# Performance work log

Hardware: AMD Instinct MI355X
Metric: run time of the kernel (lower is better)

## Reference

```python
import jax, jax.numpy as jnp
import numpy as np

N_NODES = 50000
N_EDGES = 600000
D = 128
EDGE_D = 32
N_LAYERS = 3
BN_EPS = 1e-5


def setup_inputs() -> dict:
    key = jax.random.key(0)
    ks = jax.random.split(key, 8)
    x = jax.random.normal(ks[0], (N_NODES, D), dtype=jnp.float32)
    edge_index = jax.random.randint(ks[1], (2, N_EDGES), 0, N_NODES, dtype=jnp.int64)
    edge_attr = jax.random.normal(ks[2], (N_EDGES, EDGE_D), dtype=jnp.float32)
    W_lin = jax.random.normal(ks[3], (N_LAYERS, EDGE_D, D), dtype=jnp.float32) * 0.05
    b_lin = jnp.zeros((N_LAYERS, D), dtype=jnp.float32)
    W1 = jax.random.normal(ks[4], (N_LAYERS, D, D), dtype=jnp.float32) * 0.05
    b1 = jnp.zeros((N_LAYERS, D), dtype=jnp.float32)
    W2 = jax.random.normal(ks[5], (N_LAYERS, D, D), dtype=jnp.float32) * 0.05
    b2 = jnp.zeros((N_LAYERS, D), dtype=jnp.float32)
    gamma = jnp.ones((N_LAYERS, D), dtype=jnp.float32)
    beta = jnp.zeros((N_LAYERS, D), dtype=jnp.float32)
    return {"x": x, "edge_index": edge_index, "edge_attr": edge_attr,
            "W_lin": W_lin, "b_lin": b_lin, "W1": W1, "b1": b1,
            "W2": W2, "b2": b2, "gamma": gamma, "beta": beta}


def reference(x, edge_index, edge_attr, W_lin, b_lin, W1, b1, W2, b2, gamma, beta):
    # MPNN with GINEConv layers: for each layer,
    #   msg_e = ReLU(x[src_e] + Linear(edge_attr_e))      (PyG GINEConv edge lift)
    #   agg_i = sum over edges with dst==i of msg_e        (scatter-sum)
    #   h     = MLP((1+eps)*x + agg), eps=0
    #   x     = ReLU(BatchNorm1d(h))                       (training-mode batch stats)
    src, dst = edge_index[0], edge_index[1]
    n = x.shape[0]
    for l in range(W1.shape[0]):
        e = edge_attr @ W_lin[l] + b_lin[l]                 # [E, D]
        msg = jax.nn.relu(x[src] + e)                       # gather + fuse
        agg = jax.ops.segment_sum(msg, dst, num_segments=n)  # [N, D]
        h = x + agg                                         # eps = 0
        h = jax.nn.relu(h @ W1[l] + b1[l]) @ W2[l] + b2[l]   # GIN MLP
        mu = jnp.mean(h, axis=0)
        var = jnp.var(h, axis=0)
        h = (h - mu) * jax.lax.rsqrt(var + BN_EPS) * gamma[l] + beta[l]
        x = jax.nn.relu(h)
    return x
```

## Files before the change

kernel.cpp:

```cpp
#include <hip/hip_runtime.h>

#define D_DIM 128
#define EDGE_DIM 32
#define BN_EPS 1e-5f

typedef __attribute__((ext_vector_type(8))) _Float16 f16x8;
typedef __attribute__((ext_vector_type(2))) _Float16 half2v;
typedef __attribute__((ext_vector_type(4))) float f32x4;
typedef unsigned short ushort_t;

__device__ __forceinline__ unsigned short f2h(float f) {
    union { _Float16 h; unsigned short u; } c;
    c.h = (_Float16)f;
    return c.u;
}
__device__ __forceinline__ unsigned pk2h(float lo, float hi) {
    return (unsigned)f2h(lo) | ((unsigned)f2h(hi) << 16);
}
__device__ __forceinline__ half2v asH2(unsigned u) {
    union { unsigned u; half2v h; } c;
    c.u = u;
    return c.h;
}
__device__ __forceinline__ float fdot2f(half2v a, half2v b, float c) {
#if __has_builtin(__builtin_amdgcn_fdot2)
    return __builtin_amdgcn_fdot2(a, b, c, false);
#else
    return c + (float)a.x * (float)b.x + (float)a.y * (float)b.y;
#endif
}

__global__ __launch_bounds__(256) void hist_kernel(
    const int* __restrict__ dst, int* __restrict__ cnt, int E)
{
    for (int e = blockIdx.x * 256 + threadIdx.x; e < E; e += gridDim.x * 256)
        atomicAdd(&cnt[dst[e]], 1);
}

__global__ __launch_bounds__(256) void scan_local_kernel(
    const int* __restrict__ cnt, int* __restrict__ off,
    int* __restrict__ blksum, int n)
{
    __shared__ int part[256];
    const int t = threadIdx.x;
    const int base = blockIdx.x * 2048 + t * 8;
    int v[8];
    int s = 0;
#pragma unroll
    for (int j = 0; j < 8; ++j) {
        const int idx = base + j;
        const int c = (idx < n) ? cnt[idx] : 0;
        v[j] = s;
        s += c;
    }
    part[t] = s;
    __syncthreads();
    for (int d = 1; d < 256; d <<= 1) {
        const int val = (t >= d) ? part[t - d] : 0;
        __syncthreads();
        part[t] += val;
        __syncthreads();
    }
    const int texcl = (t > 0) ? part[t - 1] : 0;
#pragma unroll
    for (int j = 0; j < 8; ++j) {
        const int idx = base + j;
        if (idx < n) off[idx] = texcl + v[j];
    }
    if (t == 255) blksum[blockIdx.x] = part[255];
}

__global__ __launch_bounds__(64) void scan_tops_kernel(
    int* __restrict__ blksum, int* __restrict__ off, int n, int B)
{
    if (threadIdx.x == 0) {
        int run = 0;
        for (int b = 0; b < B; ++b) {
            const int v = blksum[b];
            blksum[b] = run;
            run += v;
        }
        off[n] = run;
    }
}

__global__ __launch_bounds__(256) void scan_add_kernel(
    int* __restrict__ off, int* __restrict__ cur,
    const int* __restrict__ blksum, int n)
{
    const int base = blockIdx.x * 2048;
    const int add = blksum[blockIdx.x];
    for (int j = threadIdx.x; j < 2048; j += 256) {
        const int i = base + j;
        if (i < n) {
            const int v = off[i] + add;
            off[i] = v;
            cur[i] = v;
        }
    }
}

__global__ __launch_bounds__(256) void scatter_kernel(
    const int* __restrict__ src, const int* __restrict__ dst,
    int* __restrict__ cur, int* __restrict__ srcs,
    int* __restrict__ csr_eid, int E)
{
    for (int e = blockIdx.x * 256 + threadIdx.x; e < E; e += gridDim.x * 256) {
        const int p = atomicAdd(&cur[dst[e]], 1);
        srcs[p]    = src[e];
        csr_eid[p] = e;
    }
}

__global__ __launch_bounds__(256) void ea_permute_kernel(
    const float* __restrict__ ea, const int* __restrict__ csr_eid,
    uint4* __restrict__ ea16q, int E)
{
    const int idx = blockIdx.x * 256 + threadIdx.x;
    const int p = idx >> 2;
    if (p >= E) return;
    const int q = idx & 3;
    const int eid = csr_eid[p];
    const float4 a = *(const float4*)(ea + (size_t)eid * EDGE_DIM + q * 8);
    const float4 b = *(const float4*)(ea + (size_t)eid * EDGE_DIM + q * 8 + 4);
    uint4 o;
    o.x = pk2h(a.x, a.y); o.y = pk2h(a.z, a.w);
    o.z = pk2h(b.x, b.y); o.w = pk2h(b.z, b.w);
    ea16q[(size_t)p * 4 + q] = o;
}

__global__ __launch_bounds__(256) void wl_build_kernel(
    const float* __restrict__ Wl, unsigned* __restrict__ wl16d)
{
#pragma unroll
    for (int r = 0; r < 8; ++r) {
        const int idx = r * 256 + threadIdx.x;
        const int kp = idx >> 7, c = idx & 127;
        wl16d[idx] = pk2h(Wl[(2 * kp) * D_DIM + c], Wl[(2 * kp + 1) * D_DIM + c]);
    }
}

template<int XFORM>
__global__ __launch_bounds__(256) void xprep_kernel(
    const float* __restrict__ h, const float* __restrict__ scsh,
    uint2* __restrict__ x16q, int M)
{
    __shared__ float sc[128], sh[128];
    if (XFORM) {
        if (threadIdx.x < 128) {
            sc[threadIdx.x] = scsh[threadIdx.x];
            sh[threadIdx.x] = scsh[128 + threadIdx.x];
        }
        __syncthreads();
    }
    const int total = M * 32;
    for (int i = blockIdx.x * 256 + threadIdx.x; i < total; i += gridDim.x * 256) {
        float4 v = ((const float4*)h)[i];
        if (XFORM) {
            const int c = (i & 31) * 4;
            v.x = fmaxf(fmaf(v.x, sc[c + 0], sh[c + 0]), 0.f);
            v.y = fmaxf(fmaf(v.y, sc[c + 1], sh[c + 1]), 0.f);
            v.z = fmaxf(fmaf(v.z, sc[c + 2], sh[c + 2]), 0.f);
            v.w = fmaxf(fmaf(v.w, sc[c + 3], sh[c + 3]), 0.f);
        }
        uint2 o; o.x = pk2h(v.x, v.y); o.y = pk2h(v.z, v.w);
        x16q[i] = o;
    }
}

__global__ __launch_bounds__(256) void edge_agg_kernel(
    const unsigned* __restrict__ x16d,
    const int*      __restrict__ srcs,
    const uint4*    __restrict__ ea16q,
    const int*      __restrict__ row_off,
    const unsigned* __restrict__ wl16d,
    const float*    __restrict__ bl,
    float*          __restrict__ agg,
    int nNodes)
{
    const int lane = threadIdx.x & 63;
    const int wid  = threadIdx.x >> 6;

    unsigned wA[16], wB[16];
#pragma unroll
    for (int kp = 0; kp < 16; ++kp) {
        const uint2 w2 = *(const uint2*)(wl16d + kp * 128 + 2 * lane);
        wA[kp] = w2.x; wB[kp] = w2.y;
    }
    const float b0 = bl[2 * lane];
    const float b1 = bl[2 * lane + 1];

    const int stride = gridDim.x * 4;
    for (int node = blockIdx.x * 4 + wid; node < nNodes; node += stride) {
        const int beg = __builtin_amdgcn_readfirstlane(row_off[node]);
        const int end = __builtin_amdgcn_readfirstlane(row_off[node + 1]);
        float acc0 = 0.f, acc1 = 0.f;

        auto edge_body = [&](int p) {
            const int s = srcs[p];
            const uint4 q0 = ea16q[(size_t)p * 4 + 0];
            const uint4 q1 = ea16q[(size_t)p * 4 + 1];
            const uint4 q2 = ea16q[(size_t)p * 4 + 2];
            const uint4 q3 = ea16q[(size_t)p * 4 + 3];
            const unsigned xd = x16d[(size_t)s * 64 + lane];
            const unsigned aw[16] = {q0.x, q0.y, q0.z, q0.w,
                                     q1.x, q1.y, q1.z, q1.w,
                                     q2.x, q2.y, q2.z, q2.w,
                                     q3.x, q3.y, q3.z, q3.w};
            float e0 = b0, e1 = b1;
#pragma unroll
            for (int kp = 0; kp < 16; ++kp) {
                e0 = fdot2f(asH2(aw[kp]), asH2(wA[kp]), e0);
                e1 = fdot2f(asH2(aw[kp]), asH2(wB[kp]), e1);
            }
            const half2v xh = asH2(xd);
            acc0 += fmaxf((float)xh.x + e0, 0.f);
            acc1 += fmaxf((float)xh.y + e1, 0.f);
        };

        int j = beg;
        if ((end - beg) & 1) { edge_body(j); ++j; }
#pragma unroll 1
        for (; j < end; j += 2) {
            edge_body(j);
            edge_body(j + 1);
        }
        *(float2*)(agg + (size_t)node * D_DIM + 2 * lane) = make_float2(acc0, acc1);
    }
}

__global__ __launch_bounds__(256) void gemm1_kernel(
    const unsigned* __restrict__ x16d,
    const float* __restrict__ agg,
    const float* __restrict__ W,
    const float* __restrict__ bias,
    ushort_t* __restrict__ h1,
    int M)
{
    __shared__ char ATb[128 * 256];
    __shared__ char WTb[128 * 256];
    const int tid = threadIdx.x;
    const int m0  = blockIdx.x * 128;

#pragma unroll
    for (int i = 0; i < 16; ++i) {
        const int idx = i * 256 + tid;
        const int r = idx >> 5, c4 = idx & 31;
        const int row = m0 + r;
        f32x4 v = {0.f, 0.f, 0.f, 0.f};
        if (row < M) {
            const uint2 xv = *(const uint2*)(x16d + (size_t)row * 64 + c4 * 2);
            const f32x4 g  = *(const f32x4*)(agg + (size_t)row * 128 + c4 * 4);
            const half2v xa = asH2(xv.x), xb = asH2(xv.y);
            v[0] = (float)xa.x + g[0];
            v[1] = (float)xa.y + g[1];
            v[2] = (float)xb.x + g[2];
            v[3] = (float)xb.y + g[3];
        }
        uint2 p; p.x = pk2h(v[0], v[1]); p.y = pk2h(v[2], v[3]);
        *(uint2*)(ATb + r * 256 + ((c4 * 8) ^ ((r & 7) << 4))) = p;
    }
#pragma unroll
    for (int i = 0; i < 8; ++i) {
        const int c4 = (tid >> 6) + 4 * i;
        const int kp = tid & 63;
        const f32x4 wa = *(const f32x4*)(W + (size_t)(2 * kp) * 128 + c4 * 4);
        const f32x4 wb = *(const f32x4*)(W + (size_t)(2 * kp + 1) * 128 + c4 * 4);
#pragma unroll
        for (int j = 0; j < 4; ++j) {
            const int col = c4 * 4 + j;
            *(unsigned*)(WTb + col * 256 + ((kp * 4) ^ ((col & 7) << 4))) = pk2h(wa[j], wb[j]);
        }
    }
    __syncthreads();

    const int lane = tid & 63;
    const int w    = tid >> 6;
    const int fr   = lane & 15;
    const int fg   = lane >> 4;

    f32x4 acc[2][8];
#pragma unroll
    for (int a = 0; a < 2; ++a)
#pragma unroll
        for (int b = 0; b < 8; ++b) acc[a][b] = (f32x4){0.f, 0.f, 0.f, 0.f};

    const int ar0 = w * 32 + fr;
    const int asz = (ar0 & 7) << 4;
#pragma unroll
    for (int ks = 0; ks < 4; ++ks) {
        const int kb = ks * 64 + fg * 16;
        const f16x8 a0 = *(const f16x8*)(ATb + ar0 * 256 + (kb ^ asz));
        const f16x8 a1 = *(const f16x8*)(ATb + (ar0 + 16) * 256 + (kb ^ asz));
#pragma unroll
        for (int cb = 0; cb < 8; ++cb) {
            const int col = cb * 16 + fr;
            const f16x8 b = *(const f16x8*)(WTb + col * 256 + (kb ^ ((col & 7) << 4)));
            acc[0][cb] = __builtin_amdgcn_mfma_f32_16x16x32_f16(a0, b, acc[0][cb], 0, 0, 0);
            acc[1][cb] = __builtin_amdgcn_mfma_f32_16x16x32_f16(a1, b, acc[1][cb], 0, 0, 0);
        }
    }

    float bv[8];
#pragma unroll
    for (int cb = 0; cb < 8; ++cb) bv[cb] = bias[cb * 16 + fr];
#pragma unroll
    for (int rf = 0; rf < 2; ++rf) {
        const int r0 = m0 + w * 32 + rf * 16 + fg * 4;
#pragma unroll
        for (int cb = 0; cb < 8; ++cb) {
            const int col = cb * 16 + fr;
#pragma unroll
            for (int j = 0; j < 4; ++j) {
                const int row = r0 + j;
                if (row < M) {
                    const float v = fmaxf(acc[rf][cb][j] + bv[cb], 0.f);
                    h1[(size_t)row * 128 + col] = f2h(v);
                }
            }
        }
    }
}

__global__ __launch_bounds__(256) void gemm2_kernel(
    const ushort_t* __restrict__ h1,
    const float* __restrict__ W,
    const float* __restrict__ bias,
    float* __restrict__ C,
    float* __restrict__ sums,
    int M)
{
    __shared__ char ATb[128 * 256];
    __shared__ char WTb[128 * 256];
    __shared__ float bsum[256];
    const int tid = threadIdx.x;
    const int m0  = blockIdx.x * 128;

    bsum[tid] = 0.f;

#pragma unroll
    for (int i = 0; i < 8; ++i) {
        const int idx = i * 256 + tid;
        const int r = idx >> 4, c8 = idx & 15;
        const int row = m0 + r;
        uint4 v = make_uint4(0u, 0u, 0u, 0u);
        if (row < M) v = *(const uint4*)(h1 + (size_t)row * 128 + c8 * 8);
        *(uint4*)(ATb + r * 256 + ((c8 * 16) ^ ((r & 7) << 4))) = v;
    }
#pragma unroll
    for (int i = 0; i < 8; ++i) {
        const int c4 = (tid >> 6) + 4 * i;
        const int kp = tid & 63;
        const f32x4 wa = *(const f32x4*)(W + (size_t)(2 * kp) * 128 + c4 * 4);
        const f32x4 wb = *(const f32x4*)(W + (size_t)(2 * kp + 1) * 128 + c4 * 4);
#pragma unroll
        for (int j = 0; j < 4; ++j) {
            const int col = c4 * 4 + j;
            *(unsigned*)(WTb + col * 256 + ((kp * 4) ^ ((col & 7) << 4))) = pk2h(wa[j], wb[j]);
        }
    }
    __syncthreads();

    const int lane = tid & 63;
    const int w    = tid >> 6;
    const int fr   = lane & 15;
    const int fg   = lane >> 4;

    f32x4 acc[2][8];
#pragma unroll
    for (int a = 0; a < 2; ++a)
#pragma unroll
        for (int b = 0; b < 8; ++b) acc[a][b] = (f32x4){0.f, 0.f, 0.f, 0.f};

    const int ar0 = w * 32 + fr;
    const int asz = (ar0 & 7) << 4;
#pragma unroll
    for (int ks = 0; ks < 4; ++ks) {
        const int kb = ks * 64 + fg * 16;
        const f16x8 a0 = *(const f16x8*)(ATb + ar0 * 256 + (kb ^ asz));
        const f16x8 a1 = *(const f16x8*)(ATb + (ar0 + 16) * 256 + (kb ^ asz));
#pragma unroll
        for (int cb = 0; cb < 8; ++cb) {
            const int col = cb * 16 + fr;
            const f16x8 b = *(const f16x8*)(WTb + col * 256 + (kb ^ ((col & 7) << 4)));
            acc[0][cb] = __builtin_amdgcn_mfma_f32_16x16x32_f16(a0, b, acc[0][cb], 0, 0, 0);
            acc[1][cb] = __builtin_amdgcn_mfma_f32_16x16x32_f16(a1, b, acc[1][cb], 0, 0, 0);
        }
    }

    float bv[8];
#pragma unroll
    for (int cb = 0; cb < 8; ++cb) bv[cb] = bias[cb * 16 + fr];
    float s[8], q[8];
#pragma unroll
    for (int cb = 0; cb < 8; ++cb) { s[cb] = 0.f; q[cb] = 0.f; }

#pragma unroll
    for (int rf = 0; rf < 2; ++rf) {
        const int r0 = m0 + w * 32 + rf * 16 + fg * 4;
#pragma unroll
        for (int cb = 0; cb < 8; ++cb) {
            const int col = cb * 16 + fr;
#pragma unroll
            for (int j = 0; j < 4; ++j) {
                const int row = r0 + j;
                if (row < M) {
                    const float v = acc[rf][cb][j] + bv[cb];
                    C[(size_t)row * 128 + col] = v;
                    s[cb] += v;
                    q[cb] += v * v;
                }
            }
        }
    }
#pragma unroll
    for (int cb = 0; cb < 8; ++cb) {
        float ss = s[cb]; ss += __shfl_down(ss, 32); ss += __shfl_down(ss, 16);
        float qq = q[cb]; qq += __shfl_down(qq, 32); qq += __shfl_down(qq, 16);
        if (lane < 16) {
            atomicAdd(&bsum[cb * 16 + lane], ss);
            atomicAdd(&bsum[128 + cb * 16 + lane], qq);
        }
    }
    __syncthreads();
    unsafeAtomicAdd(&sums[tid], bsum[tid]);
}

__global__ __launch_bounds__(128) void bn_finalize_kernel(
    const float* __restrict__ sums,
    const float* __restrict__ gamma, const float* __restrict__ beta,
    float* __restrict__ scsh, float invM)
{
    const int c = threadIdx.x;
    const float mu  = sums[c] * invM;
    const float var = sums[128 + c] * invM - mu * mu;
    const float sc  = gamma[c] * rsqrtf(var + BN_EPS);
    scsh[c]       = sc;
    scsh[128 + c] = beta[c] - mu * sc;
}

__global__ __launch_bounds__(256) void bn_apply_final(
    float* __restrict__ h, const float* __restrict__ scsh, int M)
{
    __shared__ float sc[128], sh[128];
    if (threadIdx.x < 128) {
        sc[threadIdx.x] = scsh[threadIdx.x];
        sh[threadIdx.x] = scsh[128 + threadIdx.x];
    }
    __syncthreads();
    const size_t total = (size_t)M * D_DIM / 4;
    for (size_t i = (size_t)blockIdx.x * 256 + threadIdx.x; i < total;
         i += (size_t)gridDim.x * 256) {
        float4 v = ((const float4*)h)[i];
        const int cb = ((int)(i & 31)) * 4;
        v.x = fmaxf(fmaf(v.x, sc[cb + 0], sh[cb + 0]), 0.f);
        v.y = fmaxf(fmaf(v.y, sc[cb + 1], sh[cb + 1]), 0.f);
        v.z = fmaxf(fmaf(v.z, sc[cb + 2], sh[cb + 2]), 0.f);
        v.w = fmaxf(fmaf(v.w, sc[cb + 3], sh[cb + 3]), 0.f);
        ((float4*)h)[i] = v;
    }
}

extern "C" void kernel_launch(void* const* d_in, const int* in_sizes, int n_in,
                              void* d_out, int out_size, void* d_ws, size_t ws_size,
                              hipStream_t stream)
{
    const float* x_in  = (const float*)d_in[0];
    const int*   ei    = (const int*)  d_in[1];
    const float* ea    = (const float*)d_in[2];
    const float* W_lin = (const float*)d_in[3];
    const float* b_lin = (const float*)d_in[4];
    const float* W1    = (const float*)d_in[5];
    const float* b1    = (const float*)d_in[6];
    const float* W2    = (const float*)d_in[7];
    const float* b2    = (const float*)d_in[8];
    const float* gamma = (const float*)d_in[9];
    const float* beta  = (const float*)d_in[10];

    const int N = in_sizes[0] / D_DIM;
    const int E = in_sizes[2] / EDGE_DIM;
    const int L = in_sizes[3] / (EDGE_DIM * D_DIM);

    const int* src = ei;
    const int* dst = ei + E;

    float* out = (float*)d_out;

    char* wp = (char*)d_ws;
    auto take = [&wp](size_t bytes) {
        char* r = wp;
        wp += (bytes + 15) & ~(size_t)15;
        return r;
    };
    float*     agg     = (float*)    take((size_t)N * D_DIM * 4);
    ushort_t*  h1      = (ushort_t*) take((size_t)N * D_DIM * 2);
    unsigned*  x16d    = (unsigned*) take((size_t)N * D_DIM * 2);
    float*     sums    = (float*)    take(256 * 4);
    float*     scsh    = (float*)    take(256 * 4);
    unsigned*  wl16d   = (unsigned*) take(16 * 128 * 4);
    int*       cnt     = (int*)      take((size_t)N * 4);
    int*       row_off = (int*)      take((size_t)(N + 1) * 4);
    int*       cur     = (int*)      take((size_t)N * 4);
    int*       blksum  = (int*)      take(256 * 4);
    int*       srcs    = (int*)      take((size_t)E * 4);
    int*       csr_eid = (int*)      take((size_t)E * 4);
    uint4*     ea16q   = (uint4*)    take((size_t)E * 64);

    const int gemmBlocks = (N + 127) / 128;
    const int scanBlocks = (N + 2047) / 2048;

    hipMemsetAsync(cnt, 0, (size_t)N * sizeof(int), stream);
    hist_kernel<<<1024, 256, 0, stream>>>(dst, cnt, E);
    scan_local_kernel<<<scanBlocks, 256, 0, stream>>>(cnt, row_off, blksum, N);
    scan_tops_kernel<<<1, 64, 0, stream>>>(blksum, row_off, N, scanBlocks);
    scan_add_kernel<<<scanBlocks, 256, 0, stream>>>(row_off, cur, blksum, N);
    scatter_kernel<<<1024, 256, 0, stream>>>(src, dst, cur, srcs, csr_eid, E);
    ea_permute_kernel<<<(E * 4 + 255) / 256, 256, 0, stream>>>(ea, csr_eid, ea16q, E);

    for (int l = 0; l < L; ++l) {
        hipMemsetAsync(sums, 0, 256 * sizeof(float), stream);

        const float* Wl_l = W_lin + (size_t)l * EDGE_DIM * D_DIM;
        const float* bl_l = b_lin + (size_t)l * D_DIM;
        const float* W1_l = W1 + (size_t)l * D_DIM * D_DIM;
        const float* b1_l = b1 + (size_t)l * D_DIM;
        const float* W2_l = W2 + (size_t)l * D_DIM * D_DIM;
        const float* b2_l = b2 + (size_t)l * D_DIM;

        if (l == 0)
            xprep_kernel<0><<<2048, 256, 0, stream>>>(x_in, nullptr, (uint2*)x16d, N);
        else
            xprep_kernel<1><<<2048, 256, 0, stream>>>(out, scsh, (uint2*)x16d, N);

        wl_build_kernel<<<1, 256, 0, stream>>>(Wl_l, wl16d);

        edge_agg_kernel<<<2048, 256, 0, stream>>>(
            x16d, srcs, ea16q, row_off, wl16d, bl_l, agg, N);

        gemm1_kernel<<<gemmBlocks, 256, 0, stream>>>(
            x16d, agg, W1_l, b1_l, h1, N);

        gemm2_kernel<<<gemmBlocks, 256, 0, stream>>>(
            h1, W2_l, b2_l, out, sums, N);

        bn_finalize_kernel<<<1, 128, 0, stream>>>(
            sums, gamma + (size_t)l * D_DIM, beta + (size_t)l * D_DIM,
            scsh, 1.f / (float)N);
    }

    bn_apply_final<<<2048, 256, 0, stream>>>(out, scsh, N);
}
```

Baseline: 480.6 us.

## Fuse GIN MLP GEMMs, fuse CSR scatter with edge-attr conversion, fp16 pre-BN storage

The two MLP GEMMs become one kernel that keeps the ReLU hidden activations in shared memory instead of writing and rereading an fp16 h1 buffer. The scatter and edge-attribute permute/convert kernels merge, which removes the csr_eid array and one pass. The pre-BN output is now stored as fp16 and the BN apply is fused into the next layer's x16 prep, with a separate fp32 final apply. The edge loop is unrolled by four. Storing pre-BN activations in fp16 lowers precision, and the per-edge scatter now reads edge rows uncoalesced from each thread.

```diff
diff --git a/kernel.cpp b/kernel.cpp
--- a/kernel.cpp
+++ b/kernel.cpp
@@ -100,33 +100,26 @@
     }
 }
 
-__global__ __launch_bounds__(256) void scatter_kernel(
+__global__ __launch_bounds__(256) void scatter_conv_kernel(
     const int* __restrict__ src, const int* __restrict__ dst,
+    const float* __restrict__ ea,
     int* __restrict__ cur, int* __restrict__ srcs,
-    int* __restrict__ csr_eid, int E)
+    uint4* __restrict__ ea16q, int E)
 {
     for (int e = blockIdx.x * 256 + threadIdx.x; e < E; e += gridDim.x * 256) {
         const int p = atomicAdd(&cur[dst[e]], 1);
-        srcs[p]    = src[e];
-        csr_eid[p] = e;
-    }
-}
-
-__global__ __launch_bounds__(256) void ea_permute_kernel(
-    const float* __restrict__ ea, const int* __restrict__ csr_eid,
-    uint4* __restrict__ ea16q, int E)
-{
-    const int idx = blockIdx.x * 256 + threadIdx.x;
-    const int p = idx >> 2;
-    if (p >= E) return;
-    const int q = idx & 3;
-    const int eid = csr_eid[p];
-    const float4 a = *(const float4*)(ea + (size_t)eid * EDGE_DIM + q * 8);
-    const float4 b = *(const float4*)(ea + (size_t)eid * EDGE_DIM + q * 8 + 4);
-    uint4 o;
-    o.x = pk2h(a.x, a.y); o.y = pk2h(a.z, a.w);
-    o.z = pk2h(b.x, b.y); o.w = pk2h(b.z, b.w);
-    ea16q[(size_t)p * 4 + q] = o;
+        srcs[p] = src[e];
+        const float* __restrict__ er = ea + (size_t)e * EDGE_DIM;
+#pragma unroll
+        for (int q = 0; q < 4; ++q) {
+            const float4 a = *(const float4*)(er + q * 8);
+            const float4 b = *(const float4*)(er + q * 8 + 4);
+            uint4 o;
+            o.x = pk2h(a.x, a.y); o.y = pk2h(a.z, a.w);
+            o.z = pk2h(b.x, b.y); o.w = pk2h(b.z, b.w);
+            ea16q[(size_t)p * 4 + q] = o;
+        }
+    }
 }
 
 __global__ __launch_bounds__(256) void wl_build_kernel(
@@ -140,31 +133,44 @@
     }
 }
 
-template<int XFORM>
-__global__ __launch_bounds__(256) void xprep_kernel(
-    const float* __restrict__ h, const float* __restrict__ scsh,
-    uint2* __restrict__ x16q, int M)
-{
-    __shared__ float sc[128], sh[128];
-    if (XFORM) {
-        if (threadIdx.x < 128) {
-            sc[threadIdx.x] = scsh[threadIdx.x];
-            sh[threadIdx.x] = scsh[128 + threadIdx.x];
-        }
-        __syncthreads();
-    }
+__global__ __launch_bounds__(256) void xprep0_kernel(
+    const float* __restrict__ h, uint2* __restrict__ x16q, int M)
+{
     const int total = M * 32;
     for (int i = blockIdx.x * 256 + threadIdx.x; i < total; i += gridDim.x * 256) {
-        float4 v = ((const float4*)h)[i];
-        if (XFORM) {
-            const int c = (i & 31) * 4;
-            v.x = fmaxf(fmaf(v.x, sc[c + 0], sh[c + 0]), 0.f);
-            v.y = fmaxf(fmaf(v.y, sc[c + 1], sh[c + 1]), 0.f);
-            v.z = fmaxf(fmaf(v.z, sc[c + 2], sh[c + 2]), 0.f);
-            v.w = fmaxf(fmaf(v.w, sc[c + 3], sh[c + 3]), 0.f);
-        }
+        const float4 v = ((const float4*)h)[i];
         uint2 o; o.x = pk2h(v.x, v.y); o.y = pk2h(v.z, v.w);
         x16q[i] = o;
+    }
+}
+
+template<int OUTF32>
+__global__ __launch_bounds__(256) void apply_kernel(
+    const ushort_t* __restrict__ h16, const float* __restrict__ scsh,
+    uint2* __restrict__ x16q, float* __restrict__ outp, int M)
+{
+    __shared__ float sc[128], sh[128];
+    if (threadIdx.x < 128) {
+        sc[threadIdx.x] = scsh[threadIdx.x];
+        sh[threadIdx.x] = scsh[128 + threadIdx.x];
+    }
+    __syncthreads();
+    const int total = M * 32;
+    for (int i = blockIdx.x * 256 + threadIdx.x; i < total; i += gridDim.x * 256) {
+        const uint2 hv = *(const uint2*)(h16 + (size_t)i * 4);
+        const half2v a = asH2(hv.x), b = asH2(hv.y);
+        const int c = (i & 31) * 4;
+        const float v0 = fmaxf(fmaf((float)a.x, sc[c + 0], sh[c + 0]), 0.f);
+        const float v1 = fmaxf(fmaf((float)a.y, sc[c + 1], sh[c + 1]), 0.f);
+        const float v2 = fmaxf(fmaf((float)b.x, sc[c + 2], sh[c + 2]), 0.f);
+        const float v3 = fmaxf(fmaf((float)b.y, sc[c + 3], sh[c + 3]), 0.f);
+        if (OUTF32) {
+            f32x4 o = {v0, v1, v2, v3};
+            *(f32x4*)(outp + (size_t)i * 4) = o;
+        } else {
+            uint2 o; o.x = pk2h(v0, v1); o.y = pk2h(v2, v3);
+            x16q[i] = o;
+        }
     }
 }
 
@@ -219,28 +225,38 @@
         };
 
         int j = beg;
-        if ((end - beg) & 1) { edge_body(j); ++j; }
+        const int head = (end - beg) & 3;
 #pragma unroll 1
-        for (; j < end; j += 2) {
+        for (int t = 0; t < head; ++t) { edge_body(j); ++j; }
+#pragma unroll 1
+        for (; j < end; j += 4) {
             edge_body(j);
             edge_body(j + 1);
+            edge_body(j + 2);
+            edge_body(j + 3);
         }
         *(float2*)(agg + (size_t)node * D_DIM + 2 * lane) = make_float2(acc0, acc1);
     }
 }
 
-__global__ __launch_bounds__(256) void gemm1_kernel(
+__global__ __launch_bounds__(256) void fused_mlp_kernel(
     const unsigned* __restrict__ x16d,
     const float* __restrict__ agg,
-    const float* __restrict__ W,
-    const float* __restrict__ bias,
-    ushort_t* __restrict__ h1,
+    const float* __restrict__ W1,
+    const float* __restrict__ b1,
+    const float* __restrict__ W2,
+    const float* __restrict__ b2,
+    ushort_t* __restrict__ h16,
+    float* __restrict__ sums,
     int M)
 {
     __shared__ char ATb[128 * 256];
     __shared__ char WTb[128 * 256];
+    __shared__ float bsum[256];
     const int tid = threadIdx.x;
     const int m0  = blockIdx.x * 128;
+
+    bsum[tid] = 0.f;
 
 #pragma unroll
     for (int i = 0; i < 16; ++i) {
@@ -264,8 +280,8 @@
     for (int i = 0; i < 8; ++i) {
         const int c4 = (tid >> 6) + 4 * i;
         const int kp = tid & 63;
-        const f32x4 wa = *(const f32x4*)(W + (size_t)(2 * kp) * 128 + c4 * 4);
-        const f32x4 wb = *(const f32x4*)(W + (size_t)(2 * kp + 1) * 128 + c4 * 4);
+        const f32x4 wa = *(const f32x4*)(W1 + (size_t)(2 * kp) * 128 + c4 * 4);
+        const f32x4 wb = *(const f32x4*)(W1 + (size_t)(2 * kp + 1) * 128 + c4 * 4);
 #pragma unroll
         for (int j = 0; j < 4; ++j) {
             const int col = c4 * 4 + j;
@@ -278,6 +294,8 @@
     const int w    = tid >> 6;
     const int fr   = lane & 15;
     const int fg   = lane >> 4;
+    const int ar0  = w * 32 + fr;
+    const int asz  = (ar0 & 7) << 4;
 
     f32x4 acc[2][8];
 #pragma unroll
@@ -285,8 +303,6 @@
 #pragma unroll
         for (int b = 0; b < 8; ++b) acc[a][b] = (f32x4){0.f, 0.f, 0.f, 0.f};
 
-    const int ar0 = w * 32 + fr;
-    const int asz = (ar0 & 7) << 4;
 #pragma unroll
     for (int ks = 0; ks < 4; ++ks) {
         const int kb = ks * 64 + fg * 16;
@@ -300,80 +316,45 @@
             acc[1][cb] = __builtin_amdgcn_mfma_f32_16x16x32_f16(a1, b, acc[1][cb], 0, 0, 0);
         }
     }
-
-    float bv[8];
-#pragma unroll
-    for (int cb = 0; cb < 8; ++cb) bv[cb] = bias[cb * 16 + fr];
-#pragma unroll
-    for (int rf = 0; rf < 2; ++rf) {
-        const int r0 = m0 + w * 32 + rf * 16 + fg * 4;
-#pragma unroll
-        for (int cb = 0; cb < 8; ++cb) {
-            const int col = cb * 16 + fr;
-#pragma unroll
-            for (int j = 0; j < 4; ++j) {
-                const int row = r0 + j;
-                if (row < M) {
-                    const float v = fmaxf(acc[rf][cb][j] + bv[cb], 0.f);
-                    h1[(size_t)row * 128 + col] = f2h(v);
+    __syncthreads();
+
+    {
+        float b1v[8];
+#pragma unroll
+        for (int cb = 0; cb < 8; ++cb) b1v[cb] = b1[cb * 16 + fr];
+#pragma unroll
+        for (int rf = 0; rf < 2; ++rf) {
+            const int rb = w * 32 + rf * 16 + fg * 4;
+#pragma unroll
+            for (int cb = 0; cb < 8; ++cb) {
+                const int c = cb * 16 + fr;
+#pragma unroll
+                for (int j = 0; j < 4; ++j) {
+                    const int r = rb + j;
+                    const float v = fmaxf(acc[rf][cb][j] + b1v[cb], 0.f);
+                    *(ushort_t*)(ATb + r * 256 + ((c * 2) ^ ((r & 7) << 4))) = f2h(v);
                 }
             }
         }
-    }
-}
-
-__global__ __launch_bounds__(256) void gemm2_kernel(
-    const ushort_t* __restrict__ h1,
-    const float* __restrict__ W,
-    const float* __restrict__ bias,
-    float* __restrict__ C,
-    float* __restrict__ sums,
-    int M)
-{
-    __shared__ char ATb[128 * 256];
-    __shared__ char WTb[128 * 256];
-    __shared__ float bsum[256];
-    const int tid = threadIdx.x;
-    const int m0  = blockIdx.x * 128;
-
-    bsum[tid] = 0.f;
-
-#pragma unroll
-    for (int i = 0; i < 8; ++i) {
-        const int idx = i * 256 + tid;
-        const int r = idx >> 4, c8 = idx & 15;
-        const int row = m0 + r;
-        uint4 v = make_uint4(0u, 0u, 0u, 0u);
-        if (row < M) v = *(const uint4*)(h1 + (size_t)row * 128 + c8 * 8);
-        *(uint4*)(ATb + r * 256 + ((c8 * 16) ^ ((r & 7) << 4))) = v;
     }
 #pragma unroll
     for (int i = 0; i < 8; ++i) {
         const int c4 = (tid >> 6) + 4 * i;
         const int kp = tid & 63;
-        const f32x4 wa = *(const f32x4*)(W + (size_t)(2 * kp) * 128 + c4 * 4);
-        const f32x4 wb = *(const f32x4*)(W + (size_t)(2 * kp + 1) * 128 + c4 * 4);
+        const f32x4 wa = *(const f32x4*)(W2 + (size_t)(2 * kp) * 128 + c4 * 4);
+        const f32x4 wb = *(const f32x4*)(W2 + (size_t)(2 * kp + 1) * 128 + c4 * 4);
 #pragma unroll
         for (int j = 0; j < 4; ++j) {
             const int col = c4 * 4 + j;
             *(unsigned*)(WTb + col * 256 + ((kp * 4) ^ ((col & 7) << 4))) = pk2h(wa[j], wb[j]);
         }
     }
+#pragma unroll
+    for (int a = 0; a < 2; ++a)
+#pragma unroll
+        for (int b = 0; b < 8; ++b) acc[a][b] = (f32x4){0.f, 0.f, 0.f, 0.f};
     __syncthreads();
 
-    const int lane = tid & 63;
-    const int w    = tid >> 6;
-    const int fr   = lane & 15;
-    const int fg   = lane >> 4;
-
-    f32x4 acc[2][8];
-#pragma unroll
-    for (int a = 0; a < 2; ++a)
-#pragma unroll
-        for (int b = 0; b < 8; ++b) acc[a][b] = (f32x4){0.f, 0.f, 0.f, 0.f};
-
-    const int ar0 = w * 32 + fr;
-    const int asz = (ar0 & 7) << 4;
 #pragma unroll
     for (int ks = 0; ks < 4; ++ks) {
         const int kb = ks * 64 + fg * 16;
@@ -388,9 +369,9 @@
         }
     }
 
-    float bv[8];
-#pragma unroll
-    for (int cb = 0; cb < 8; ++cb) bv[cb] = bias[cb * 16 + fr];
+    float b2v[8];
+#pragma unroll
+    for (int cb = 0; cb < 8; ++cb) b2v[cb] = b2[cb * 16 + fr];
     float s[8], q[8];
 #pragma unroll
     for (int cb = 0; cb < 8; ++cb) { s[cb] = 0.f; q[cb] = 0.f; }
@@ -405,8 +386,8 @@
             for (int j = 0; j < 4; ++j) {
                 const int row = r0 + j;
                 if (row < M) {
-                    const float v = acc[rf][cb][j] + bv[cb];
-                    C[(size_t)row * 128 + col] = v;
+                    const float v = acc[rf][cb][j] + b2v[cb];
+                    h16[(size_t)row * 128 + col] = f2h(v);
                     s[cb] += v;
                     q[cb] += v * v;
                 }
@@ -437,28 +418,6 @@
     const float sc  = gamma[c] * rsqrtf(var + BN_EPS);
     scsh[c]       = sc;
     scsh[128 + c] = beta[c] - mu * sc;
-}
-
-__global__ __launch_bounds__(256) void bn_apply_final(
-    float* __restrict__ h, const float* __restrict__ scsh, int M)
-{
-    __shared__ float sc[128], sh[128];
-    if (threadIdx.x < 128) {
-        sc[threadIdx.x] = scsh[threadIdx.x];
-        sh[threadIdx.x] = scsh[128 + threadIdx.x];
-    }
-    __syncthreads();
-    const size_t total = (size_t)M * D_DIM / 4;
-    for (size_t i = (size_t)blockIdx.x * 256 + threadIdx.x; i < total;
-         i += (size_t)gridDim.x * 256) {
-        float4 v = ((const float4*)h)[i];
-        const int cb = ((int)(i & 31)) * 4;
-        v.x = fmaxf(fmaf(v.x, sc[cb + 0], sh[cb + 0]), 0.f);
-        v.y = fmaxf(fmaf(v.y, sc[cb + 1], sh[cb + 1]), 0.f);
-        v.z = fmaxf(fmaf(v.z, sc[cb + 2], sh[cb + 2]), 0.f);
-        v.w = fmaxf(fmaf(v.w, sc[cb + 3], sh[cb + 3]), 0.f);
-        ((float4*)h)[i] = v;
-    }
 }
 
 extern "C" void kernel_launch(void* const* d_in, const int* in_sizes, int n_in,
@@ -493,7 +452,7 @@
         return r;
     };
     float*     agg     = (float*)    take((size_t)N * D_DIM * 4);
-    ushort_t*  h1      = (ushort_t*) take((size_t)N * D_DIM * 2);
+    ushort_t*  h16     = (ushort_t*) take((size_t)N * D_DIM * 2);
     unsigned*  x16d    = (unsigned*) take((size_t)N * D_DIM * 2);
     float*     sums    = (float*)    take(256 * 4);
     float*     scsh    = (float*)    take(256 * 4);
@@ -503,7 +462,6 @@
     int*       cur     = (int*)      take((size_t)N * 4);
     int*       blksum  = (int*)      take(256 * 4);
     int*       srcs    = (int*)      take((size_t)E * 4);
-    int*       csr_eid = (int*)      take((size_t)E * 4);
     uint4*     ea16q   = (uint4*)    take((size_t)E * 64);
 
     const int gemmBlocks = (N + 127) / 128;
@@ -514,8 +472,7 @@
     scan_local_kernel<<<scanBlocks, 256, 0, stream>>>(cnt, row_off, blksum, N);
     scan_tops_kernel<<<1, 64, 0, stream>>>(blksum, row_off, N, scanBlocks);
     scan_add_kernel<<<scanBlocks, 256, 0, stream>>>(row_off, cur, blksum, N);
-    scatter_kernel<<<1024, 256, 0, stream>>>(src, dst, cur, srcs, csr_eid, E);
-    ea_permute_kernel<<<(E * 4 + 255) / 256, 256, 0, stream>>>(ea, csr_eid, ea16q, E);
+    scatter_conv_kernel<<<1024, 256, 0, stream>>>(src, dst, ea, cur, srcs, ea16q, E);
 
     for (int l = 0; l < L; ++l) {
         hipMemsetAsync(sums, 0, 256 * sizeof(float), stream);
@@ -528,25 +485,22 @@
         const float* b2_l = b2 + (size_t)l * D_DIM;
 
         if (l == 0)
-            xprep_kernel<0><<<2048, 256, 0, stream>>>(x_in, nullptr, (uint2*)x16d, N);
+            xprep0_kernel<<<1024, 256, 0, stream>>>(x_in, (uint2*)x16d, N);
         else
-            xprep_kernel<1><<<2048, 256, 0, stream>>>(out, scsh, (uint2*)x16d, N);
+            apply_kernel<0><<<1024, 256, 0, stream>>>(h16, scsh, (uint2*)x16d, nullptr, N);
 
         wl_build_kernel<<<1, 256, 0, stream>>>(Wl_l, wl16d);
 
         edge_agg_kernel<<<2048, 256, 0, stream>>>(
             x16d, srcs, ea16q, row_off, wl16d, bl_l, agg, N);
 
-        gemm1_kernel<<<gemmBlocks, 256, 0, stream>>>(
-            x16d, agg, W1_l, b1_l, h1, N);
-
-        gemm2_kernel<<<gemmBlocks, 256, 0, stream>>>(
-            h1, W2_l, b2_l, out, sums, N);
+        fused_mlp_kernel<<<gemmBlocks, 256, 0, stream>>>(
+            x16d, agg, W1_l, b1_l, W2_l, b2_l, h16, sums, N);
 
         bn_finalize_kernel<<<1, 128, 0, stream>>>(
             sums, gamma + (size_t)l * D_DIM, beta + (size_t)l * D_DIM,
             scsh, 1.f / (float)N);
     }
 
-    bn_apply_final<<<2048, 256, 0, stream>>>(out, scsh, N);
-}
+    apply_kernel<1><<<1024, 256, 0, stream>>>(h16, scsh, nullptr, out, N);
+}
```

Measured after the change: 433.1 us. 1.11x faster.
